# Optimization experiments

Hardware: AMD Instinct MI355X
Metric: run time of the kernel (lower is better)

## Reference

```python
import jax, jax.numpy as jnp
import numpy as np
from jax import lax

DIM = 64
HEADS = 4
B, Q, V = 8, 128, 128


def _modrelu(z, b):
    m = jnp.abs(z)
    return z * (jax.nn.relu(m + b) / (m + 1e-5))


def _eunn_unitary(h, th1, ph1, th2, ph2, om):
    # tunable-style EUNN, capacity 2: even-pair rotations, odd-pair rotations, diagonal phase
    d = h.shape[-1]
    # layer 1: pairs (0,1),(2,3),...
    hp = h.reshape(*h.shape[:-1], d // 2, 2)
    a, b = hp[..., 0], hp[..., 1]
    c1, s1, e1 = jnp.cos(th1), jnp.sin(th1), jnp.exp(1j * ph1)
    h = jnp.stack([e1 * (c1 * a - s1 * b), s1 * a + c1 * b], -1).reshape(h.shape)
    # layer 2: pairs (1,2),(3,4),...,(d-3,d-2); endpoints pass through
    mid = h[..., 1:d - 1].reshape(*h.shape[:-1], d // 2 - 1, 2)
    a, b = mid[..., 0], mid[..., 1]
    c2, s2, e2 = jnp.cos(th2), jnp.sin(th2), jnp.exp(1j * ph2)
    mid2 = jnp.stack([e2 * (c2 * a - s2 * b), s2 * a + c2 * b], -1).reshape(*h.shape[:-1], d - 2)
    h = jnp.concatenate([h[..., :1], mid2, h[..., d - 1:]], -1)
    return h * jnp.exp(1j * om)


def _forward(queries, values, U_re, U_im, bias, theta1, phi1, theta2, phi2, omega, W_dense, b_dense):
    Bq, Qq, d = queries.shape
    Vv = values.shape[1]
    # quadratic (query, value) expansion -> [B*Q, V, 2d]
    dq = jnp.broadcast_to(queries[:, :, None, :], (Bq, Qq, Vv, d))
    dv = jnp.broadcast_to(values[:, None, :, :], (Bq, Qq, Vv, d))
    x = jnp.concatenate([dq, dv], -1).reshape(Bq * Qq, Vv, 2 * d)
    U = (U_re + 1j * U_im)  # [H, 2d, d] complex input kernel per head
    Ux = jnp.einsum('nvi,hij->hvnj', x.astype(jnp.complex64), U)  # [H, V, N, d]

    def run_head(Ux_h, t1, p1, t2, p2, om, bh):
        def step(h, u):
            h2 = _modrelu(_eunn_unitary(h, t1, p1, t2, p2, om) + u, bh)
            return h2, None
        h0 = jnp.zeros(Ux_h.shape[1:], dtype=jnp.complex64)  # [N, d]
        hT, _ = lax.scan(step, h0, Ux_h)
        return hT  # final state, as Keras RNN with return_sequences=False

    outs = jax.vmap(run_head)(Ux, theta1, phi1, theta2, phi2, omega, bias)  # [H, N, d]
    acc = jnp.real(outs).transpose(1, 0, 2).reshape(Bq * Qq, HEADS * d)
    y = acc @ W_dense + b_dense
    return y.reshape(Bq, Qq, d)


def setup_inputs() -> dict:
    key = jax.random.key(0)
    ks = jax.random.split(key, 12)
    pi = np.pi
    return {
        'queries': jax.random.normal(ks[0], (B, Q, DIM), jnp.float32),
        'values': jax.random.normal(ks[1], (B, V, DIM), jnp.float32),
        'U_re': jax.random.normal(ks[2], (HEADS, 2 * DIM, DIM), jnp.float32) * (1.0 / np.sqrt(2 * DIM)),
        'U_im': jax.random.normal(ks[3], (HEADS, 2 * DIM, DIM), jnp.float32) * (1.0 / np.sqrt(2 * DIM)),
        'bias': jax.random.normal(ks[4], (HEADS, DIM), jnp.float32) * 0.01,
        'theta1': jax.random.uniform(ks[5], (HEADS, DIM // 2), jnp.float32, -pi, pi),
        'phi1': jax.random.uniform(ks[6], (HEADS, DIM // 2), jnp.float32, -pi, pi),
        'theta2': jax.random.uniform(ks[7], (HEADS, DIM // 2 - 1), jnp.float32, -pi, pi),
        'phi2': jax.random.uniform(ks[8], (HEADS, DIM // 2 - 1), jnp.float32, -pi, pi),
        'omega': jax.random.uniform(ks[9], (HEADS, DIM), jnp.float32, -pi, pi),
        'W_dense': jax.random.normal(ks[10], (HEADS * DIM, DIM), jnp.float32) * (1.0 / np.sqrt(HEADS * DIM)),
        'b_dense': jnp.zeros((DIM,), jnp.float32),
    }


def reference(queries, values, U_re, U_im, bias, theta1, phi1, theta2, phi2, omega, W_dense, b_dense):
    return _forward(queries, values, U_re, U_im, bias, theta1, phi1, theta2, phi2, omega, W_dense, b_dense)
```

## Files before the change

kernel.cpp:

```cpp
#include <hip/hip_runtime.h>
#include <math.h>

#define DIM 64
#define HEADS 4
#define BB 8
#define QQ 128
#define VV 128
#define NN (BB*QQ)

typedef float f2 __attribute__((ext_vector_type(2)));
typedef float f4 __attribute__((ext_vector_type(4)));

template <int CTRL>
__device__ __forceinline__ float dppf(float x) {
    return __int_as_float(__builtin_amdgcn_update_dpp(
        0, __float_as_int(x), CTRL, 0xF, 0xF, true));
}
#define SWAP1 0xB1
#define WSHR1 0x138
#define WSHL1 0x130

__device__ __forceinline__ f2 b2(float s) { f2 r; r.x = s; r.y = s; return r; }
#define SW(v) __builtin_shufflevector((v), (v), 1, 0)
#define FMA2(a, b, c) __builtin_elementwise_fma((a), (b), (c))

__global__ __launch_bounds__(256) void k_av(const float* __restrict__ values,
                                            const float* __restrict__ U_re,
                                            const float* __restrict__ U_im,
                                            const float* __restrict__ bias,
                                            const float* __restrict__ theta1,
                                            const float* __restrict__ phi1,
                                            const float* __restrict__ theta2,
                                            const float* __restrict__ phi2,
                                            const float* __restrict__ omega,
                                            f4* __restrict__ AvP,
                                            float* __restrict__ Coef) {
    int tid = blockIdx.x * blockDim.x + threadIdx.x;
    int w = tid >> 6;
    int j = tid & 63;
    int h = w >> 9;
    int rp = w & 511;
    int r0 = rp << 1;
    const float* vrow = values + r0 * DIM;
    const float* ur = U_re + (h * 2 * DIM + DIM) * DIM + j;
    const float* ui = U_im + (h * 2 * DIM + DIM) * DIM + j;
    f2 a0 = 0.f, a1 = 0.f;
    #pragma unroll 8
    for (int i = 0; i < DIM; ++i) {
        f2 u; u.x = ur[i * DIM]; u.y = ui[i * DIM];
        a0 += vrow[i] * u;
        a1 += vrow[DIM + i] * u;
    }
    f4 o; o.x = a0.x; o.y = a0.y; o.z = a1.x; o.w = a1.y;
    AvP[(h * 512 + rp) * 64 + j] = o;

    if (blockIdx.x == 0) {
        int t = threadIdx.x;
        int hh = t >> 6, jj = t & 63;
        int k1 = jj >> 1;
        float th1 = theta1[hh * 32 + k1], ph1 = phi1[hh * 32 + k1];
        float C1 = cosf(th1), s1v = sinf(th1);
        float S1, E1r, E1i;
        if ((jj & 1) == 0) { S1 = -s1v; E1r = cosf(ph1); E1i = sinf(ph1); }
        else               { S1 =  s1v; E1r = 1.f;       E1i = 0.f;       }
        float C2, SL, SR, p2r, p2i;
        if (jj == 0 || jj == 63) {
            C2 = 1.f; SL = 0.f; SR = 0.f; p2r = 1.f; p2i = 0.f;
        } else {
            int k2 = (jj - 1) >> 1;
            float th2 = theta2[hh * 31 + k2], ph2 = phi2[hh * 31 + k2];
            float c2 = cosf(th2), s2 = sinf(th2);
            if (jj & 1) { C2 = c2; SL = -s2; SR = 0.f; p2r = cosf(ph2); p2i = sinf(ph2); }
            else        { C2 = c2; SR =  s2; SL = 0.f; p2r = 1.f;       p2i = 0.f;      }
        }
        float om = omega[hh * 64 + jj];
        float eor = cosf(om), eoi = sinf(om);
        float PHr = p2r * eor - p2i * eoi;
        float PHi = p2r * eoi + p2i * eor;
        Coef[0 * 256 + t] = C1;
        Coef[1 * 256 + t] = S1;
        Coef[2 * 256 + t] = E1r;
        Coef[3 * 256 + t] = E1i;
        Coef[4 * 256 + t] = C2;
        Coef[5 * 256 + t] = SL;
        Coef[6 * 256 + t] = SR;
        Coef[7 * 256 + t] = PHr;
        Coef[8 * 256 + t] = PHi;
        Coef[9 * 256 + t] = bias[hh * 64 + jj];
    }
}

__global__ __launch_bounds__(256, 4) void k_rnn_dense(
        const float* __restrict__ queries,
        const float* __restrict__ U_re,
        const float* __restrict__ U_im,
        const float* __restrict__ Coef,
        const f4* __restrict__ AvP,
        const float* __restrict__ W_dense,
        const float* __restrict__ b_dense,
        float* __restrict__ y) {
    int n = blockIdx.x;
    int t = threadIdx.x;
    int h = t >> 6;
    int j = t & 63;
    int b = n >> 7;

    float C1  = Coef[0 * 256 + t];
    float S1  = Coef[1 * 256 + t];
    float E1r = Coef[2 * 256 + t];
    float E1i = Coef[3 * 256 + t];
    float C2  = Coef[4 * 256 + t];
    float SL  = Coef[5 * 256 + t];
    float SR  = Coef[6 * 256 + t];
    float PHr = Coef[7 * 256 + t];
    float PHi = Coef[8 * 256 + t];
    float bj  = Coef[9 * 256 + t];

    f2 C1p = b2(C1), S1p = b2(S1), E1rp = b2(E1r);
    f2 E1in; E1in.x = -E1i; E1in.y = E1i;
    f2 C2p = b2(C2), SLp = b2(SL), SRp = b2(SR), PHrp = b2(PHr);
    f2 PHin; PHin.x = -PHi; PHin.y = PHi;

    const float* q0 = queries + n * DIM;
    const float* ur = U_re + (h * 2 * DIM) * DIM + j;
    const float* ui = U_im + (h * 2 * DIM) * DIM + j;
    f2 uq = 0.f;
    #pragma unroll 8
    for (int i = 0; i < DIM; ++i) {
        f2 u; u.x = ur[i * DIM]; u.y = ui[i * DIM];
        uq = FMA2(b2(q0[i]), u, uq);
    }

    f2 hS = 0.f;
    auto step = [&](f2 av) {
        f2 uv = uq + av;
        f2 p; p.x = dppf<SWAP1>(hS.x); p.y = dppf<SWAP1>(hS.y);
        f2 tp = FMA2(C1p, hS, S1p * p);
        f2 T  = FMA2(E1rp, tp, E1in * SW(tp));
        f2 L; L.x = dppf<WSHL1>(T.x); L.y = dppf<WSHL1>(T.y);
        f2 R; R.x = dppf<WSHR1>(T.x); R.y = dppf<WSHR1>(T.y);
        f2 sp = FMA2(C2p, T, FMA2(SLp, L, SRp * R));
        f2 z  = FMA2(PHrp, sp, FMA2(PHin, SW(sp), uv));
        float q2 = fmaf(z.x, z.x, fmaf(z.y, z.y, 1e-10f));
        float rs = __builtin_amdgcn_rsqf(q2);
        float sc = fmaxf(fmaf(bj, rs, 1.f), 0.f);
        hS = z * b2(sc);
    };

    const f4* p = AvP + (h * 512 + b * 64) * 64 + j;
    f4 buf[4], nxt[4];
    #pragma unroll
    for (int k = 0; k < 4; ++k) buf[k] = p[k * 64];

    for (int w = 0; w < 16; ++w) {
        const f4* pn = p + ((w < 15) ? 4 * 64 : 0);
        #pragma unroll
        for (int k = 0; k < 4; ++k) nxt[k] = pn[k * 64];
        p = pn;
        #pragma unroll
        for (int k = 0; k < 4; ++k) {
            f2 a; a.x = buf[k].x; a.y = buf[k].y;
            step(a);
            f2 c; c.x = buf[k].z; c.y = buf[k].w;
            step(c);
        }
        #pragma unroll
        for (int k = 0; k < 4; ++k) buf[k] = nxt[k];
    }

    __shared__ float s_acc[HEADS * DIM];
    __shared__ float s_part[256];
    s_acc[h * 64 + j] = hS.x;
    __syncthreads();

    {
        int qq = t >> 6, jj = t & 63;
        const float* Wp = W_dense + (qq * 64) * DIM + jj;
        const float* ap = &s_acc[qq * 64];
        float part = 0.f;
        #pragma unroll 8
        for (int k = 0; k < 64; ++k)
            part = fmaf(ap[k], Wp[k * DIM], part);
        s_part[t] = part;
    }
    __syncthreads();
    if (t < 64) {
        y[n * DIM + t] = b_dense[t] + s_part[t] + s_part[64 + t]
                       + s_part[128 + t] + s_part[192 + t];
    }
}

extern "C" void kernel_launch(void* const* d_in, const int* in_sizes, int n_in,
                              void* d_out, int out_size, void* d_ws, size_t ws_size,
                              hipStream_t stream) {
    const float* queries = (const float*)d_in[0];
    const float* values  = (const float*)d_in[1];
    const float* U_re    = (const float*)d_in[2];
    const float* U_im    = (const float*)d_in[3];
    const float* bias    = (const float*)d_in[4];
    const float* theta1  = (const float*)d_in[5];
    const float* phi1    = (const float*)d_in[6];
    const float* theta2  = (const float*)d_in[7];
    const float* phi2    = (const float*)d_in[8];
    const float* omega   = (const float*)d_in[9];
    const float* W_dense = (const float*)d_in[10];
    const float* b_dense = (const float*)d_in[11];
    float* y = (float*)d_out;

    f4* AvP = (f4*)d_ws;
    float* Coef = (float*)((char*)d_ws + HEADS * 512 * 64 * sizeof(f4));

    k_av<<<512, 256, 0, stream>>>(values, U_re, U_im, bias, theta1, phi1,
                                  theta2, phi2, omega, AvP, Coef);
    k_rnn_dense<<<1024, 256, 0, stream>>>(queries, U_re, U_im, Coef, AvP,
                                          W_dense, b_dense, y);
}
```

Before: 115.9 us.

## Stage AvP chunks into LDS with async global_load_lds double buffering

The per-thread register prefetch of AvP is replaced by direct global-to-LDS loads into a 64 KB double buffer. Each 8-timestep chunk is staged while the previous one is computed, with a block barrier between chunks. The dense-stage scratch arrays now reuse this LDS region, and the occupancy hint drops from 4 to 2 blocks. The goal is to hide global-load latency behind the recurrence, at the cost of lower occupancy, block-wide barriers coupling the four head wavefronts, and dependence on the barrier waiting for the async loads to finish.

```diff
diff --git a/kernel.cpp b/kernel.cpp
--- a/kernel.cpp
+++ b/kernel.cpp
@@ -23,6 +23,12 @@
 __device__ __forceinline__ f2 b2(float s) { f2 r; r.x = s; r.y = s; return r; }
 #define SW(v) __builtin_shufflevector((v), (v), 1, 0)
 #define FMA2(a, b, c) __builtin_elementwise_fma((a), (b), (c))
+
+__device__ __forceinline__ void gl_lds16(const f4* g, f4* l) {
+    __builtin_amdgcn_global_load_lds(
+        (const __attribute__((address_space(1))) void*)g,
+        (__attribute__((address_space(3))) void*)l, 16, 0, 0);
+}
 
 __global__ __launch_bounds__(256) void k_av(const float* __restrict__ values,
                                             const float* __restrict__ U_re,
@@ -90,7 +96,7 @@
     }
 }
 
-__global__ __launch_bounds__(256, 4) void k_rnn_dense(
+__global__ __launch_bounds__(256, 2) void k_rnn_dense(
         const float* __restrict__ queries,
         const float* __restrict__ U_re,
         const float* __restrict__ U_im,
@@ -99,11 +105,22 @@
         const float* __restrict__ W_dense,
         const float* __restrict__ b_dense,
         float* __restrict__ y) {
+    __shared__ f4 sAv[2][HEADS][8][64];
     int n = blockIdx.x;
     int t = threadIdx.x;
     int h = t >> 6;
     int j = t & 63;
     int b = n >> 7;
+
+    const f4* gsrc = AvP + (h * 512 + b * 64) * 64 + j;
+    auto stage = [&](int pb, int c) {
+        const f4* g = gsrc + c * 8 * 64;
+        #pragma unroll
+        for (int pp = 0; pp < 8; ++pp)
+            gl_lds16(g + pp * 64, &sAv[pb][h][pp][0]);
+    };
+
+    stage(0, 0);
 
     float C1  = Coef[0 * 256 + t];
     float S1  = Coef[1 * 256 + t];
@@ -147,29 +164,26 @@
         hS = z * b2(sc);
     };
 
-    const f4* p = AvP + (h * 512 + b * 64) * 64 + j;
-    f4 buf[4], nxt[4];
-    #pragma unroll
-    for (int k = 0; k < 4; ++k) buf[k] = p[k * 64];
-
-    for (int w = 0; w < 16; ++w) {
-        const f4* pn = p + ((w < 15) ? 4 * 64 : 0);
+    __syncthreads();
+
+    for (int c = 0; c < 8; ++c) {
+        int cb = c & 1;
+        if (c < 7) stage(cb ^ 1, c + 1);
+        f4 ch[8];
         #pragma unroll
-        for (int k = 0; k < 4; ++k) nxt[k] = pn[k * 64];
-        p = pn;
+        for (int pp = 0; pp < 8; ++pp) ch[pp] = sAv[cb][h][pp][j];
         #pragma unroll
-        for (int k = 0; k < 4; ++k) {
-            f2 a; a.x = buf[k].x; a.y = buf[k].y;
+        for (int pp = 0; pp < 8; ++pp) {
+            f2 a; a.x = ch[pp].x; a.y = ch[pp].y;
             step(a);
-            f2 c; c.x = buf[k].z; c.y = buf[k].w;
-            step(c);
+            f2 d; d.x = ch[pp].z; d.y = ch[pp].w;
+            step(d);
         }
-        #pragma unroll
-        for (int k = 0; k < 4; ++k) buf[k] = nxt[k];
-    }
-
-    __shared__ float s_acc[HEADS * DIM];
-    __shared__ float s_part[256];
+        __syncthreads();
+    }
+
+    float* s_acc = (float*)&sAv[0][0][0][0];
+    float* s_part = s_acc + 256;
     s_acc[h * 64 + j] = hS.x;
     __syncthreads();
 
```

Result: slower. 120.3 us (+3.8%).

## Process four query rows per block with interleaved independent RNN chains

Applied to the files above, without the earlier changes.

Each block now handles four consecutive query rows instead of one, running four independent recurrent state chains per thread that share the same Av loads and coefficients. This reuses the AvP stream across four rows and gives ILP to hide the serial dependency latency of DPP and rsq in each step. The trade is a grid cut from 1024 to 256 blocks (one per CU on a 256-CU part) with a relaxed launch bound, so occupancy drops to about one block per CU and higher register use.

```diff
diff --git a/kernel.cpp b/kernel.cpp
--- a/kernel.cpp
+++ b/kernel.cpp
@@ -90,7 +90,7 @@
     }
 }
 
-__global__ __launch_bounds__(256, 4) void k_rnn_dense(
+__global__ __launch_bounds__(256, 1) void k_rnn_dense(
         const float* __restrict__ queries,
         const float* __restrict__ U_re,
         const float* __restrict__ U_im,
@@ -99,11 +99,12 @@
         const float* __restrict__ W_dense,
         const float* __restrict__ b_dense,
         float* __restrict__ y) {
-    int n = blockIdx.x;
+    int m = blockIdx.x;
+    int n0 = m << 2;
     int t = threadIdx.x;
     int h = t >> 6;
     int j = t & 63;
-    int b = n >> 7;
+    int b = n0 >> 7;
 
     float C1  = Coef[0 * 256 + t];
     float S1  = Coef[1 * 256 + t];
@@ -121,18 +122,21 @@
     f2 C2p = b2(C2), SLp = b2(SL), SRp = b2(SR), PHrp = b2(PHr);
     f2 PHin; PHin.x = -PHi; PHin.y = PHi;
 
-    const float* q0 = queries + n * DIM;
+    const float* q0 = queries + n0 * DIM;
     const float* ur = U_re + (h * 2 * DIM) * DIM + j;
     const float* ui = U_im + (h * 2 * DIM) * DIM + j;
-    f2 uq = 0.f;
+    f2 uq0 = 0.f, uq1 = 0.f, uq2 = 0.f, uq3 = 0.f;
     #pragma unroll 8
     for (int i = 0; i < DIM; ++i) {
         f2 u; u.x = ur[i * DIM]; u.y = ui[i * DIM];
-        uq = FMA2(b2(q0[i]), u, uq);
-    }
-
-    f2 hS = 0.f;
-    auto step = [&](f2 av) {
+        uq0 = FMA2(b2(q0[i]), u, uq0);
+        uq1 = FMA2(b2(q0[DIM + i]), u, uq1);
+        uq2 = FMA2(b2(q0[2 * DIM + i]), u, uq2);
+        uq3 = FMA2(b2(q0[3 * DIM + i]), u, uq3);
+    }
+
+    f2 h0 = 0.f, h1 = 0.f, h2 = 0.f, h3 = 0.f;
+    auto step1 = [&](f2& hS, const f2& uq, const f2& av) {
         f2 uv = uq + av;
         f2 p; p.x = dppf<SWAP1>(hS.x); p.y = dppf<SWAP1>(hS.y);
         f2 tp = FMA2(C1p, hS, S1p * p);
@@ -146,6 +150,12 @@
         float sc = fmaxf(fmaf(bj, rs, 1.f), 0.f);
         hS = z * b2(sc);
     };
+    auto step4 = [&](f2 av) {
+        step1(h0, uq0, av);
+        step1(h1, uq1, av);
+        step1(h2, uq2, av);
+        step1(h3, uq3, av);
+    };
 
     const f4* p = AvP + (h * 512 + b * 64) * 64 + j;
     f4 buf[4], nxt[4];
@@ -160,33 +170,49 @@
         #pragma unroll
         for (int k = 0; k < 4; ++k) {
             f2 a; a.x = buf[k].x; a.y = buf[k].y;
-            step(a);
-            f2 c; c.x = buf[k].z; c.y = buf[k].w;
-            step(c);
+            step4(a);
+            f2 d; d.x = buf[k].z; d.y = buf[k].w;
+            step4(d);
         }
         #pragma unroll
         for (int k = 0; k < 4; ++k) buf[k] = nxt[k];
     }
 
-    __shared__ float s_acc[HEADS * DIM];
-    __shared__ float s_part[256];
-    s_acc[h * 64 + j] = hS.x;
+    __shared__ float s_acc[4][HEADS * DIM];
+    __shared__ float s_part[4][256];
+    s_acc[0][h * 64 + j] = h0.x;
+    s_acc[1][h * 64 + j] = h1.x;
+    s_acc[2][h * 64 + j] = h2.x;
+    s_acc[3][h * 64 + j] = h3.x;
     __syncthreads();
 
     {
         int qq = t >> 6, jj = t & 63;
         const float* Wp = W_dense + (qq * 64) * DIM + jj;
-        const float* ap = &s_acc[qq * 64];
-        float part = 0.f;
+        const float* a0 = &s_acc[0][qq * 64];
+        const float* a1 = &s_acc[1][qq * 64];
+        const float* a2 = &s_acc[2][qq * 64];
+        const float* a3 = &s_acc[3][qq * 64];
+        float p0 = 0.f, p1 = 0.f, p2 = 0.f, p3 = 0.f;
         #pragma unroll 8
-        for (int k = 0; k < 64; ++k)
-            part = fmaf(ap[k], Wp[k * DIM], part);
-        s_part[t] = part;
+        for (int k = 0; k < 64; ++k) {
+            float wv = Wp[k * DIM];
+            p0 = fmaf(a0[k], wv, p0);
+            p1 = fmaf(a1[k], wv, p1);
+            p2 = fmaf(a2[k], wv, p2);
+            p3 = fmaf(a3[k], wv, p3);
+        }
+        s_part[0][t] = p0;
+        s_part[1][t] = p1;
+        s_part[2][t] = p2;
+        s_part[3][t] = p3;
     }
     __syncthreads();
-    if (t < 64) {
-        y[n * DIM + t] = b_dense[t] + s_part[t] + s_part[64 + t]
-                       + s_part[128 + t] + s_part[192 + t];
+    {
+        int r = t >> 6, c = t & 63;
+        y[(n0 + r) * DIM + c] = b_dense[c]
+            + s_part[r][c] + s_part[r][64 + c]
+            + s_part[r][128 + c] + s_part[r][192 + c];
     }
 }
 
@@ -212,6 +238,6 @@
 
     k_av<<<512, 256, 0, stream>>>(values, U_re, U_im, bias, theta1, phi1,
                                   theta2, phi2, omega, AvP, Coef);
-    k_rnn_dense<<<1024, 256, 0, stream>>>(queries, U_re, U_im, Coef, AvP,
-                                          W_dense, b_dense, y);
-}
+    k_rnn_dense<<<256, 256, 0, stream>>>(queries, U_re, U_im, Coef, AvP,
+                                         W_dense, b_dense, y);
+}
```

Result: faster. 111.7 us (-3.6%).

## Process two query rows per block with SoA complex layout in RNN kernel

Applied to the files above, without the earlier changes.

Each block now handles two adjacent query rows (n0, n0+1), which share the same batch and therefore the same value-projection stream. It stores real and imaginary parts as separate f2 pairs across the two rows, so every packed FMA works on two independent recurrences and the lane-swap shufflevectors go away. The AvP loads, coefficient setup and W_dense reads are amortized over two outputs, and the grid is halved. The cost is more DPP ops per step, higher register use (launch bounds lowered to 2 blocks/CU), and fewer blocks in flight.

```diff
diff --git a/kernel.cpp b/kernel.cpp
--- a/kernel.cpp
+++ b/kernel.cpp
@@ -21,7 +21,6 @@
 #define WSHL1 0x130
 
 __device__ __forceinline__ f2 b2(float s) { f2 r; r.x = s; r.y = s; return r; }
-#define SW(v) __builtin_shufflevector((v), (v), 1, 0)
 #define FMA2(a, b, c) __builtin_elementwise_fma((a), (b), (c))
 
 __global__ __launch_bounds__(256) void k_av(const float* __restrict__ values,
@@ -90,7 +89,7 @@
     }
 }
 
-__global__ __launch_bounds__(256, 4) void k_rnn_dense(
+__global__ __launch_bounds__(256, 2) void k_rnn_dense(
         const float* __restrict__ queries,
         const float* __restrict__ U_re,
         const float* __restrict__ U_im,
@@ -99,11 +98,12 @@
         const float* __restrict__ W_dense,
         const float* __restrict__ b_dense,
         float* __restrict__ y) {
-    int n = blockIdx.x;
+    int m = blockIdx.x;
+    int n0 = m << 1;
     int t = threadIdx.x;
     int h = t >> 6;
     int j = t & 63;
-    int b = n >> 7;
+    int b = n0 >> 7;
 
     float C1  = Coef[0 * 256 + t];
     float S1  = Coef[1 * 256 + t];
@@ -116,35 +116,52 @@
     float PHi = Coef[8 * 256 + t];
     float bj  = Coef[9 * 256 + t];
 
-    f2 C1p = b2(C1), S1p = b2(S1), E1rp = b2(E1r);
-    f2 E1in; E1in.x = -E1i; E1in.y = E1i;
-    f2 C2p = b2(C2), SLp = b2(SL), SRp = b2(SR), PHrp = b2(PHr);
-    f2 PHin; PHin.x = -PHi; PHin.y = PHi;
-
-    const float* q0 = queries + n * DIM;
+    f2 C1p = b2(C1), S1p = b2(S1);
+    f2 E1rp = b2(E1r), E1ip = b2(E1i), mE1ip = b2(-E1i);
+    f2 C2p = b2(C2), SLp = b2(SL), SRp = b2(SR);
+    f2 PHrp = b2(PHr), PHip = b2(PHi), mPHip = b2(-PHi);
+    f2 bjp = b2(bj), onep = b2(1.f), epsp = b2(1e-10f), zerop = b2(0.f);
+
+    const float* q0 = queries + n0 * DIM;
+    const float* q1 = q0 + DIM;
     const float* ur = U_re + (h * 2 * DIM) * DIM + j;
     const float* ui = U_im + (h * 2 * DIM) * DIM + j;
-    f2 uq = 0.f;
+    f2 uqr = 0.f, uqi = 0.f;
     #pragma unroll 8
     for (int i = 0; i < DIM; ++i) {
-        f2 u; u.x = ur[i * DIM]; u.y = ui[i * DIM];
-        uq = FMA2(b2(q0[i]), u, uq);
-    }
-
-    f2 hS = 0.f;
-    auto step = [&](f2 av) {
-        f2 uv = uq + av;
-        f2 p; p.x = dppf<SWAP1>(hS.x); p.y = dppf<SWAP1>(hS.y);
-        f2 tp = FMA2(C1p, hS, S1p * p);
-        f2 T  = FMA2(E1rp, tp, E1in * SW(tp));
-        f2 L; L.x = dppf<WSHL1>(T.x); L.y = dppf<WSHL1>(T.y);
-        f2 R; R.x = dppf<WSHR1>(T.x); R.y = dppf<WSHR1>(T.y);
-        f2 sp = FMA2(C2p, T, FMA2(SLp, L, SRp * R));
-        f2 z  = FMA2(PHrp, sp, FMA2(PHin, SW(sp), uv));
-        float q2 = fmaf(z.x, z.x, fmaf(z.y, z.y, 1e-10f));
-        float rs = __builtin_amdgcn_rsqf(q2);
-        float sc = fmaxf(fmaf(bj, rs, 1.f), 0.f);
-        hS = z * b2(sc);
+        float u_r = ur[i * DIM], u_i = ui[i * DIM];
+        f2 a; a.x = q0[i]; a.y = q1[i];
+        uqr = FMA2(a, b2(u_r), uqr);
+        uqi = FMA2(a, b2(u_i), uqi);
+    }
+
+    f2 hr = 0.f, hi = 0.f;
+    auto step = [&](float avr, float avi) {
+        f2 uvr = uqr + b2(avr);
+        f2 uvi = uqi + b2(avi);
+        f2 pr, pi;
+        pr.x = dppf<SWAP1>(hr.x); pr.y = dppf<SWAP1>(hr.y);
+        pi.x = dppf<SWAP1>(hi.x); pi.y = dppf<SWAP1>(hi.y);
+        f2 tpr = FMA2(C1p, hr, S1p * pr);
+        f2 tpi = FMA2(C1p, hi, S1p * pi);
+        f2 Tr = FMA2(E1rp, tpr, mE1ip * tpi);
+        f2 Ti = FMA2(E1rp, tpi, E1ip * tpr);
+        f2 Lr, Li, Rr, Ri;
+        Lr.x = dppf<WSHL1>(Tr.x); Lr.y = dppf<WSHL1>(Tr.y);
+        Li.x = dppf<WSHL1>(Ti.x); Li.y = dppf<WSHL1>(Ti.y);
+        Rr.x = dppf<WSHR1>(Tr.x); Rr.y = dppf<WSHR1>(Tr.y);
+        Ri.x = dppf<WSHR1>(Ti.x); Ri.y = dppf<WSHR1>(Ti.y);
+        f2 spr = FMA2(C2p, Tr, FMA2(SLp, Lr, SRp * Rr));
+        f2 spi = FMA2(C2p, Ti, FMA2(SLp, Li, SRp * Ri));
+        f2 zr = FMA2(PHrp, spr, FMA2(mPHip, spi, uvr));
+        f2 zi = FMA2(PHrp, spi, FMA2(PHip, spr, uvi));
+        f2 q2 = FMA2(zr, zr, FMA2(zi, zi, epsp));
+        f2 rs;
+        rs.x = __builtin_amdgcn_rsqf(q2.x);
+        rs.y = __builtin_amdgcn_rsqf(q2.y);
+        f2 sc = __builtin_elementwise_max(FMA2(bjp, rs, onep), zerop);
+        hr = zr * sc;
+        hi = zi * sc;
     };
 
     const f4* p = AvP + (h * 512 + b * 64) * 64 + j;
@@ -159,34 +176,40 @@
         p = pn;
         #pragma unroll
         for (int k = 0; k < 4; ++k) {
-            f2 a; a.x = buf[k].x; a.y = buf[k].y;
-            step(a);
-            f2 c; c.x = buf[k].z; c.y = buf[k].w;
-            step(c);
+            step(buf[k].x, buf[k].y);
+            step(buf[k].z, buf[k].w);
         }
         #pragma unroll
         for (int k = 0; k < 4; ++k) buf[k] = nxt[k];
     }
 
-    __shared__ float s_acc[HEADS * DIM];
-    __shared__ float s_part[256];
-    s_acc[h * 64 + j] = hS.x;
+    __shared__ float s_acc[2][HEADS * DIM];
+    __shared__ float s_part[2][256];
+    s_acc[0][h * 64 + j] = hr.x;
+    s_acc[1][h * 64 + j] = hr.y;
     __syncthreads();
 
     {
         int qq = t >> 6, jj = t & 63;
         const float* Wp = W_dense + (qq * 64) * DIM + jj;
-        const float* ap = &s_acc[qq * 64];
-        float part = 0.f;
+        const float* a0 = &s_acc[0][qq * 64];
+        const float* a1 = &s_acc[1][qq * 64];
+        float part0 = 0.f, part1 = 0.f;
         #pragma unroll 8
-        for (int k = 0; k < 64; ++k)
-            part = fmaf(ap[k], Wp[k * DIM], part);
-        s_part[t] = part;
+        for (int k = 0; k < 64; ++k) {
+            float wv = Wp[k * DIM];
+            part0 = fmaf(a0[k], wv, part0);
+            part1 = fmaf(a1[k], wv, part1);
+        }
+        s_part[0][t] = part0;
+        s_part[1][t] = part1;
     }
     __syncthreads();
-    if (t < 64) {
-        y[n * DIM + t] = b_dense[t] + s_part[t] + s_part[64 + t]
-                       + s_part[128 + t] + s_part[192 + t];
+    if (t < 128) {
+        int r = t >> 6, c = t & 63;
+        y[(n0 + r) * DIM + c] = b_dense[c]
+            + s_part[r][c] + s_part[r][64 + c]
+            + s_part[r][128 + c] + s_part[r][192 + c];
     }
 }
 
@@ -212,6 +235,6 @@
 
     k_av<<<512, 256, 0, stream>>>(values, U_re, U_im, bias, theta1, phi1,
                                   theta2, phi2, omega, AvP, Coef);
-    k_rnn_dense<<<1024, 256, 0, stream>>>(queries, U_re, U_im, Coef, AvP,
-                                          W_dense, b_dense, y);
-}
+    k_rnn_dense<<<512, 256, 0, stream>>>(queries, U_re, U_im, Coef, AvP,
+                                         W_dense, b_dense, y);
+}
```

Result: faster. 110.2 us (-5.0%).
